# Kernel tuning notes

Hardware: AMD Instinct MI355X
Metric: run time of the kernel (lower is better)

## Reference

```python
import jax, jax.numpy as jnp
import numpy as np

FEAT_DIM = 256
NUM_HEADS = 4
GATE_HID = FEAT_DIM // 4
LN_EPS = 1e-5


def setup_inputs() -> dict:
    key = jax.random.key(0)
    ks = jax.random.split(key, 12)
    C, H = FEAT_DIM, NUM_HEADS
    s = 1.0 / np.sqrt(C)
    inp = {
        "features": jax.random.normal(ks[0], (8, 16384, C), dtype=jnp.float32),
        "view_proj_w": jax.random.normal(ks[1], (C, C), dtype=jnp.float32) * s,
        "view_proj_b": jnp.zeros((C,), dtype=jnp.float32),
        "in_proj_w": jax.random.normal(ks[2], (3 * C, C), dtype=jnp.float32) * s,
        "in_proj_b": jnp.zeros((3 * C,), dtype=jnp.float32),
        "out_proj_w": jax.random.normal(ks[3], (C, C), dtype=jnp.float32) * s,
        "out_proj_b": jnp.zeros((C,), dtype=jnp.float32),
        "gate_w1": jax.random.normal(ks[4], (GATE_HID, C), dtype=jnp.float32) * s,
        "gate_b1": jnp.zeros((GATE_HID,), dtype=jnp.float32),
        "gate_w2": jax.random.normal(ks[5], (1, GATE_HID), dtype=jnp.float32) * (1.0 / np.sqrt(GATE_HID)),
        "gate_b2": jnp.zeros((1,), dtype=jnp.float32),
        "ln_g": jnp.ones((C,), dtype=jnp.float32),
        "ln_b": jnp.zeros((C,), dtype=jnp.float32),
    }
    return inp


def reference(features, view_proj_w, view_proj_b, in_proj_w, in_proj_b,
              out_proj_w, out_proj_b, gate_w1, gate_b1, gate_w2, gate_b2,
              ln_g, ln_b):
    N, L, C = features.shape
    H = NUM_HEADS
    D = C // H

    # view embedding: scalar id/N broadcast over C, then Linear  -> [N,1,C]
    view_ids = (jnp.arange(N, dtype=features.dtype) / N)[:, None, None]  # [N,1,1]
    view_vec = jnp.broadcast_to(view_ids, (N, 1, C))
    view_info = view_vec @ view_proj_w.T + view_proj_b                    # [N,1,C]
    view_features = features + view_info                                  # [N,L,C]

    tokens = jnp.transpose(view_features, (1, 0, 2))                      # [L,N,C]

    # batched tiny cross-view self-attention: batch=L, seq=N
    qkv = tokens @ in_proj_w.T + in_proj_b                                # [L,N,3C]
    q, k, v = jnp.split(qkv, 3, axis=-1)
    q = q.reshape(L, N, H, D)
    k = k.reshape(L, N, H, D)
    v = v.reshape(L, N, H, D)
    scores = jnp.einsum("lnhd,lmhd->lhnm", q, k) / jnp.sqrt(jnp.array(D, features.dtype))
    attn = jax.nn.softmax(scores, axis=-1)                                # [L,H,N,N]
    ctx = jnp.einsum("lhnm,lmhd->lnhd", attn, v).reshape(L, N, C)
    attended = ctx @ out_proj_w.T + out_proj_b                            # [L,N,C]

    # gated softmax aggregation over views
    g = jax.nn.relu(attended @ gate_w1.T + gate_b1)                       # [L,N,C/4]
    g = jax.nn.sigmoid(g @ gate_w2.T + gate_b2)[..., 0]                   # [L,N]
    w = jax.nn.softmax(g, axis=-1)                                        # [L,N]
    fused = jnp.einsum("lnc,ln->lc", attended, w)[None]                   # [1,L,C]

    # LayerNorm over C
    mu = fused.mean(-1, keepdims=True)
    var = fused.var(-1, keepdims=True)
    fused = (fused - mu) * jax.lax.rsqrt(var + LN_EPS) * ln_g + ln_b
    return fused
```

## Files before the change

kernel.cpp:

```cpp
#include <hip/hip_runtime.h>

#define L_DIM 16384
#define C_DIM 256
#define NV 8
#define NH 4
#define DH 64
#define TL 4
#define NTHREADS 256

#define QKP 132
#define VVP 68
#define GPAD 68

typedef __attribute__((ext_vector_type(8))) _Float16 f16x8;
typedef __attribute__((ext_vector_type(4))) _Float16 f16x4;
typedef __attribute__((ext_vector_type(2))) _Float16 f16x2;
typedef __attribute__((ext_vector_type(4))) float f32x4;

union F8u { f16x8 v; f16x2 p[4]; };

__global__ void prep_kernel(const float* __restrict__ vw, const float* __restrict__ vb,
                            const float* __restrict__ w_in, const float* __restrict__ w_out,
                            const float* __restrict__ w_g1,
                            float* __restrict__ view_info, _Float16* __restrict__ win_pk,
                            _Float16* __restrict__ wout_pk, _Float16* __restrict__ wg1_pk){
  int tid = threadIdx.x, bid = blockIdx.x;
  if (bid == 0){
    int c = tid;
    const float4* vr = (const float4*)(vw + c*C_DIM);
    float rs = 0.f;
#pragma unroll 8
    for (int k = 0; k < 64; k++){ float4 x = vr[k]; rs += x.x + x.y + x.z + x.w; }
    float b = vb[c];
    for (int n = 0; n < NV; n++) view_info[n*C_DIM + c] = (n * 0.125f) * rs + b;
  }
  int gid = bid * blockDim.x + tid;
  int stride = gridDim.x * blockDim.x;
  const int NWIN = 24576, NWOUT = 8192, NWG = 2048;
  for (int f = gid; f < NWIN + NWOUT + NWG; f += stride){
    if (f < NWIN){
      int lane = f & 63, kc = (f>>6)&7, nt = (f>>9)&3, pc = f>>11;
      int p = pc % 3, h = pc / 3;
      int row = p*C_DIM + h*DH + nt*16 + (lane&15);
      int col = (lane>>4)*8 + kc*32;
      const float* src = w_in + (long)row*C_DIM + col;
      _Float16* d = win_pk + (long)f*8;
#pragma unroll
      for (int j = 0; j < 8; j++) d[j] = (_Float16)src[j];
    } else if (f < NWIN + NWOUT){
      int f2 = f - NWIN;
      int lane = f2 & 63, kc = (f2>>6)&7, nt = (f2>>9)&3, cc = f2>>11;
      int row = cc*64 + nt*16 + (lane&15);
      int col = (lane>>4)*8 + kc*32;
      const float* src = w_out + (long)row*C_DIM + col;
      _Float16* d = wout_pk + (long)f2*8;
#pragma unroll
      for (int j = 0; j < 8; j++) d[j] = (_Float16)src[j];
    } else {
      int f3 = f - NWIN - NWOUT;
      int lane = f3 & 63, kc = (f3>>6)&7, nt = (f3>>9)&3;
      int row = nt*16 + (lane&15);
      int col = (lane>>4)*8 + kc*32;
      const float* src = w_g1 + (long)row*C_DIM + col;
      _Float16* d = wg1_pk + (long)f3*8;
#pragma unroll
      for (int j = 0; j < 8; j++) d[j] = (_Float16)src[j];
    }
  }
}

__global__ __launch_bounds__(NTHREADS, 4)
void fused_kernel(const float* __restrict__ feat,
                  const float* __restrict__ view_info,
                  const _Float16* __restrict__ win,
                  const _Float16* __restrict__ wout,
                  const _Float16* __restrict__ wg1,
                  const float* __restrict__ b_in,
                  const float* __restrict__ b_out,
                  const float* __restrict__ b_g1,
                  const float* __restrict__ w2,
                  const float* __restrict__ b2,
                  const float* __restrict__ ln_g,
                  const float* __restrict__ ln_b,
                  float* __restrict__ out)
{
  extern __shared__ char smem[];
  _Float16* A   = (_Float16*)smem;
  _Float16* ctx = (_Float16*)smem;
  float*    g1s = (float*)smem;
  float* gl   = (float*)(smem + 8704);
  float* wgt  = gl + 32;
  float* red1 = wgt + 32;
  float* red2 = red1 + 128;
  float* mus  = red2 + 128;
  float* rvs  = mus + 4;
  _Float16* qk  = (_Float16*)(smem + 16384);
  _Float16* vv  = (_Float16*)(smem + 24832);
  _Float16* att = (_Float16*)(smem + 16384);

  const int tid  = threadIdx.x;
  const int wv   = tid >> 6, lane = tid & 63;
  const int quad = lane >> 4, l15 = lane & 15;

  const _Float16* wbin  = win  + (long)(wv*8)*512 + lane*8;
  const _Float16* wbout = wout + (long)(wv*32)*512 + lane*8;
  const _Float16* wbg1  = wg1  + (long)(wv*8)*512 + lane*8;

#define QSET(dst, g) do { int h_=(g)>>3, kc_=(g)&7; \
  dst[0] = *(const f16x8*)(wbin + ((h_*3+0)*32 + kc_)*512); \
  dst[1] = *(const f16x8*)(wbin + ((h_*3+1)*32 + kc_)*512); \
  dst[2] = *(const f16x8*)(wbin + ((h_*3+2)*32 + kc_)*512); } while(0)
#define OSET(dst, kc) do { \
  dst[0] = *(const f16x8*)(wbout + (0*8+(kc))*512); \
  dst[1] = *(const f16x8*)(wbout + (1*8+(kc))*512); \
  dst[2] = *(const f16x8*)(wbout + (2*8+(kc))*512); \
  dst[3] = *(const f16x8*)(wbout + (3*8+(kc))*512); } while(0)

  f16x8 wz[2][3];
  QSET(wz[0], 0);
  QSET(wz[1], 1);

  {
    int row = tid >> 3, j = tid & 7;
    int n = row & 7, lloc = row >> 3;
    long l = (long)blockIdx.x * TL + lloc;
    const float* fb = feat + ((long)n * L_DIM + l) * C_DIM + j*32;
    const float* vb = view_info + n * C_DIM + j*32;
    _Float16* arow = A + row*256;
#pragma unroll
    for (int i = 0; i < 4; i++){
      float4 x0 = *(const float4*)(fb + i*8);
      float4 x1 = *(const float4*)(fb + i*8 + 4);
      float4 v0 = *(const float4*)(vb + i*8);
      float4 v1 = *(const float4*)(vb + i*8 + 4);
      f16x8 hf;
      hf[0] = (_Float16)(x0.x+v0.x); hf[1] = (_Float16)(x0.y+v0.y);
      hf[2] = (_Float16)(x0.z+v0.z); hf[3] = (_Float16)(x0.w+v0.w);
      hf[4] = (_Float16)(x1.x+v1.x); hf[5] = (_Float16)(x1.y+v1.y);
      hf[6] = (_Float16)(x1.z+v1.z); hf[7] = (_Float16)(x1.w+v1.w);
      int s = j*4 + i;
      *(f16x8*)(arow + ((s ^ row))*8) = hf;
    }
  }
  __syncthreads();

  f16x8 wo[2][4];
  f16x8 wg[8];
  f16x8 cpk0, cpk1, cpk2;

#pragma unroll
  for (int h = 0; h < NH; h++){
    if (h) __syncthreads();
    {
      f32x4 z = {0.f,0.f,0.f,0.f};
      f32x4 acc[3][2];
#pragma unroll
      for (int p = 0; p < 3; p++){ acc[p][0] = z; acc[p][1] = z; }
#pragma unroll
      for (int kc = 0; kc < 8; kc++){
        int g = h*8 + kc;
        int s0 = quad + 4*kc;
        int r1 = 16 + l15;
        f16x8 a0 = *(const f16x8*)(A + l15*256 + ((s0 ^ l15))*8);
        f16x8 a1 = *(const f16x8*)(A + r1*256  + ((s0 ^ r1))*8);
#pragma unroll
        for (int p = 0; p < 3; p++){
          acc[p][0] = __builtin_amdgcn_mfma_f32_16x16x32_f16(wz[g&1][p], a0, acc[p][0], 0,0,0);
          acc[p][1] = __builtin_amdgcn_mfma_f32_16x16x32_f16(wz[g&1][p], a1, acc[p][1], 0,0,0);
        }
        if (g + 2 <= 31) QSET(wz[g&1], g+2);
      }
      int c4 = wv*16 + quad*4;
#pragma unroll
      for (int p = 0; p < 3; p++){
        float4 b4 = *(const float4*)(b_in + p*C_DIM + h*DH + c4);
        float bb[4] = {b4.x, b4.y, b4.z, b4.w};
        f16x4 s0, s1;
#pragma unroll
        for (int r = 0; r < 4; r++){
          s0[r] = (_Float16)(acc[p][0][r] + bb[r]);
          s1[r] = (_Float16)(acc[p][1][r] + bb[r]);
        }
        if (p < 2){
          *(f16x4*)(qk + l15*QKP      + p*64 + c4) = s0;
          *(f16x4*)(qk + (16+l15)*QKP + p*64 + c4) = s1;
        } else {
          *(f16x4*)(vv + l15*VVP      + c4) = s0;
          *(f16x4*)(vv + (16+l15)*VVP + c4) = s1;
        }
      }
    }
    __syncthreads();
    {
      if (h == 3){ OSET(wo[0], 0); OSET(wo[1], 1); }
      int nn = lane >> 3, mm = lane & 7;
      int tq = wv*8 + nn;
      const _Float16* qrow = qk + tq*QKP;
      const _Float16* krow = qk + (wv*8 + mm)*QKP + 64;
      float s = 0.f;
#pragma unroll
      for (int d8 = 0; d8 < 8; d8++){
        F8u q8, k8;
        q8.v = *(const f16x8*)(qrow + d8*8);
        k8.v = *(const f16x8*)(krow + d8*8);
#if __has_builtin(__builtin_amdgcn_fdot2)
#pragma unroll
        for (int j2 = 0; j2 < 4; j2++)
          s = __builtin_amdgcn_fdot2(q8.p[j2], k8.p[j2], s, false);
#else
#pragma unroll
        for (int j = 0; j < 8; j++) s += (float)q8.v[j] * (float)k8.v[j];
#endif
      }
      s *= 0.125f;
      float mx = s;
#pragma unroll
      for (int o = 1; o < 8; o <<= 1) mx = fmaxf(mx, __shfl_xor(mx, o));
      float e = __expf(s - mx);
      float sum = e;
#pragma unroll
      for (int o = 1; o < 8; o <<= 1) sum += __shfl_xor(sum, o);
      float attnw = e / sum;
      float c8[8] = {0,0,0,0,0,0,0,0};
#pragma unroll
      for (int mp = 0; mp < 8; mp++){
        float aw = __shfl(attnw, (nn<<3) | mp);
        f16x8 v8 = *(const f16x8*)(vv + (wv*8 + mp)*VVP + mm*8);
#pragma unroll
        for (int j = 0; j < 8; j++) c8[j] += aw * (float)v8[j];
      }
      f16x8 cp;
#pragma unroll
      for (int j = 0; j < 8; j++) cp[j] = (_Float16)c8[j];
      if (h == 0)      cpk0 = cp;
      else if (h == 1) cpk1 = cp;
      else if (h == 2) cpk2 = cp;
      else {
        _Float16* crow = ctx + tq*256;
        *(f16x8*)(crow + ((( 0 + mm) ^ tq))*8) = cpk0;
        *(f16x8*)(crow + ((( 8 + mm) ^ tq))*8) = cpk1;
        *(f16x8*)(crow + (((16 + mm) ^ tq))*8) = cpk2;
        *(f16x8*)(crow + (((24 + mm) ^ tq))*8) = cp;
      }
    }
  }
  __syncthreads();

  {
    f32x4 z = {0.f,0.f,0.f,0.f};
    f32x4 acc[4][2];
#pragma unroll
    for (int nt = 0; nt < 4; nt++){ acc[nt][0] = z; acc[nt][1] = z; }
#pragma unroll
    for (int kc = 0; kc < 8; kc++){
      int s0 = quad + 4*kc;
      int r1 = 16 + l15;
      f16x8 a0 = *(const f16x8*)(ctx + l15*256 + ((s0 ^ l15))*8);
      f16x8 a1 = *(const f16x8*)(ctx + r1*256  + ((s0 ^ r1))*8);
#pragma unroll
      for (int nt = 0; nt < 4; nt++){
        acc[nt][0] = __builtin_amdgcn_mfma_f32_16x16x32_f16(wo[kc&1][nt], a0, acc[nt][0], 0,0,0);
        acc[nt][1] = __builtin_amdgcn_mfma_f32_16x16x32_f16(wo[kc&1][nt], a1, acc[nt][1], 0,0,0);
      }
      if (kc < 6) OSET(wo[kc&1], kc+2);
    }
#pragma unroll
    for (int nt = 0; nt < 4; nt++){
      int c4 = wv*64 + nt*16 + quad*4;
      float4 b4 = *(const float4*)(b_out + c4);
      float bb[4] = {b4.x, b4.y, b4.z, b4.w};
      f16x4 s0, s1;
#pragma unroll
      for (int r = 0; r < 4; r++){
        s0[r] = (_Float16)(acc[nt][0][r] + bb[r]);
        s1[r] = (_Float16)(acc[nt][1][r] + bb[r]);
      }
      int slot = c4 >> 3, jo = c4 & 7;
      *(f16x4*)(att + l15*256      + ((slot ^ l15))*8      + jo) = s0;
      *(f16x4*)(att + (16+l15)*256 + ((slot ^ (16+l15)))*8 + jo) = s1;
    }
#pragma unroll
    for (int kc = 0; kc < 8; kc++) wg[kc] = *(const f16x8*)(wbg1 + kc*512);
  }
  __syncthreads();

  {
    f32x4 acc0 = {0.f,0.f,0.f,0.f}, acc1 = {0.f,0.f,0.f,0.f};
#pragma unroll
    for (int kc = 0; kc < 8; kc++){
      int s0 = quad + 4*kc;
      int r1 = 16 + l15;
      f16x8 a0 = *(const f16x8*)(att + l15*256 + ((s0 ^ l15))*8);
      f16x8 a1 = *(const f16x8*)(att + r1*256  + ((s0 ^ r1))*8);
      acc0 = __builtin_amdgcn_mfma_f32_16x16x32_f16(wg[kc], a0, acc0, 0,0,0);
      acc1 = __builtin_amdgcn_mfma_f32_16x16x32_f16(wg[kc], a1, acc1, 0,0,0);
    }
    int c4 = wv*16 + quad*4;
    float4 b4 = *(const float4*)(b_g1 + c4);
    float bb[4] = {b4.x, b4.y, b4.z, b4.w};
    float4 o0, o1;
    o0.x = fmaxf(acc0[0]+bb[0], 0.f); o0.y = fmaxf(acc0[1]+bb[1], 0.f);
    o0.z = fmaxf(acc0[2]+bb[2], 0.f); o0.w = fmaxf(acc0[3]+bb[3], 0.f);
    o1.x = fmaxf(acc1[0]+bb[0], 0.f); o1.y = fmaxf(acc1[1]+bb[1], 0.f);
    o1.z = fmaxf(acc1[2]+bb[2], 0.f); o1.w = fmaxf(acc1[3]+bb[3], 0.f);
    *(float4*)(g1s + l15*GPAD      + c4) = o0;
    *(float4*)(g1s + (16+l15)*GPAD + c4) = o1;
  }
  __syncthreads();

  {
    int t = tid >> 3, part = tid & 7;
    const float* g1r = g1s + t*GPAD + part*8;
    const float* w2p = w2 + part*8;
    float s = 0.f;
#pragma unroll
    for (int j = 0; j < 8; j++) s += g1r[j] * w2p[j];
    s += __shfl_xor(s, 1);
    s += __shfl_xor(s, 2);
    s += __shfl_xor(s, 4);
    if (part == 0) gl[t] = 1.f / (1.f + __expf(-(s + b2[0])));
  }
  __syncthreads();
  if (tid < 4){
    float v[8]; float mx = -1e30f;
    for (int n = 0; n < 8; n++){ v[n] = gl[tid*8+n]; mx = fmaxf(mx, v[n]); }
    float sum = 0.f;
    for (int n = 0; n < 8; n++){ v[n] = __expf(v[n]-mx); sum += v[n]; }
    float inv = 1.f/sum;
    for (int n = 0; n < 8; n++) wgt[tid*8+n] = v[n]*inv;
  }
  __syncthreads();

  float f8[8];
  const int lfl = tid >> 5, ccf = tid & 31;
  if (tid < 128){
    float wloc[8];
#pragma unroll
    for (int n = 0; n < 8; n++) wloc[n] = wgt[lfl*8+n];
#pragma unroll
    for (int j = 0; j < 8; j++) f8[j] = 0.f;
#pragma unroll
    for (int n = 0; n < 8; n++){
      int row = lfl*8 + n;
      f16x8 a8 = *(const f16x8*)(att + row*256 + ((ccf ^ row))*8);
      float aw = wloc[n];
#pragma unroll
      for (int j = 0; j < 8; j++) f8[j] += aw * (float)a8[j];
    }
    float s = 0.f, s2 = 0.f;
#pragma unroll
    for (int j = 0; j < 8; j++){ s += f8[j]; s2 += f8[j]*f8[j]; }
    red1[lfl*32 + ccf] = s;
    red2[lfl*32 + ccf] = s2;
  }
  __syncthreads();
  if (tid < 4){
    float s = 0.f, s2 = 0.f;
    for (int i = 0; i < 32; i++){ s += red1[tid*32+i]; s2 += red2[tid*32+i]; }
    float mu = s * (1.f/256.f);
    float var = s2 * (1.f/256.f) - mu*mu;
    mus[tid] = mu;
    rvs[tid] = rsqrtf(var + 1e-5f);
  }
  __syncthreads();
  if (tid < 128){
    float mu = mus[lfl], rv = rvs[lfl];
    long lg = (long)blockIdx.x * TL + lfl;
    float* op = out + lg * C_DIM + ccf*8;
    float o8[8];
#pragma unroll
    for (int j = 0; j < 8; j++){
      int c = ccf*8 + j;
      o8[j] = (f8[j]-mu)*rv*ln_g[c] + ln_b[c];
    }
    *(float4*)(op)   = make_float4(o8[0],o8[1],o8[2],o8[3]);
    *(float4*)(op+4) = make_float4(o8[4],o8[5],o8[6],o8[7]);
  }
}

extern "C" void kernel_launch(void* const* d_in, const int* in_sizes, int n_in,
                              void* d_out, int out_size, void* d_ws, size_t ws_size,
                              hipStream_t stream){
  const float* feat  = (const float*)d_in[0];
  const float* vw    = (const float*)d_in[1];
  const float* vb    = (const float*)d_in[2];
  const float* w_in  = (const float*)d_in[3];
  const float* b_in  = (const float*)d_in[4];
  const float* w_out = (const float*)d_in[5];
  const float* b_out = (const float*)d_in[6];
  const float* w_g1  = (const float*)d_in[7];
  const float* b_g1  = (const float*)d_in[8];
  const float* w2    = (const float*)d_in[9];
  const float* b2    = (const float*)d_in[10];
  const float* lng   = (const float*)d_in[11];
  const float* lnb   = (const float*)d_in[12];

  char* ws = (char*)d_ws;
  float*    view_info = (float*)ws;
  _Float16* win_pk  = (_Float16*)(ws + 8192);
  _Float16* wout_pk = (_Float16*)(ws + 401408);
  _Float16* wg1_pk  = (_Float16*)(ws + 532480);

  prep_kernel<<<256, 256, 0, stream>>>(vw, vb, w_in, w_out, w_g1,
                                       view_info, win_pk, wout_pk, wg1_pk);
  fused_kernel<<<L_DIM/TL, NTHREADS, 32768, stream>>>(
      feat, view_info, win_pk, wout_pk, wg1_pk,
      b_in, b_out, b_g1, w2, b2, lng, lnb, (float*)d_out);
}
```

Before: 434.9 us.

## Double tokens per block to 8 with 512 threads and two row-pair wave groups

Each block now handles 8 sequence positions (64 token rows) with 8 waves, split into two 32-row groups that share the same column-tile weight fragments. Shared memory doubles to 64 KB, and the swizzle is adjusted to use the row index modulo 32. The out-projection and gate weight loads move out of the attention loop into their own phases, with an extra barrier added. The goal is fewer blocks and better amortized weight fetches per block, at the cost of higher LDS use, which may reduce occupancy.

```diff
diff --git a/kernel.cpp b/kernel.cpp
--- a/kernel.cpp
+++ b/kernel.cpp
@@ -5,8 +5,8 @@
 #define NV 8
 #define NH 4
 #define DH 64
-#define TL 4
-#define NTHREADS 256
+#define TL 8
+#define NTHREADS 512
 
 #define QKP 132
 #define VVP 68
@@ -88,23 +88,26 @@
   _Float16* A   = (_Float16*)smem;
   _Float16* ctx = (_Float16*)smem;
   float*    g1s = (float*)smem;
-  float* gl   = (float*)(smem + 8704);
-  float* wgt  = gl + 32;
-  float* red1 = wgt + 32;
-  float* red2 = red1 + 128;
-  float* mus  = red2 + 128;
-  float* rvs  = mus + 4;
-  _Float16* qk  = (_Float16*)(smem + 16384);
-  _Float16* vv  = (_Float16*)(smem + 24832);
-  _Float16* att = (_Float16*)(smem + 16384);
+  float* gl   = (float*)(smem + 17408);
+  float* wgt  = gl + 64;
+  float* red1 = wgt + 64;
+  float* red2 = red1 + 256;
+  float* mus  = red2 + 256;
+  float* rvs  = mus + 8;
+  _Float16* qk  = (_Float16*)(smem + 32768);
+  _Float16* vv  = (_Float16*)(smem + 49664);
+  _Float16* att = (_Float16*)(smem + 32768);
 
   const int tid  = threadIdx.x;
   const int wv   = tid >> 6, lane = tid & 63;
   const int quad = lane >> 4, l15 = lane & 15;
-
-  const _Float16* wbin  = win  + (long)(wv*8)*512 + lane*8;
-  const _Float16* wbout = wout + (long)(wv*32)*512 + lane*8;
-  const _Float16* wbg1  = wg1  + (long)(wv*8)*512 + lane*8;
+  const int rp   = wv >> 2, ct = wv & 3;
+  const int r0   = rp*32 + l15;
+  const int r1   = rp*32 + 16 + l15;
+
+  const _Float16* wbin  = win  + (long)(ct*8)*512 + lane*8;
+  const _Float16* wbout = wout + (long)(ct*32)*512 + lane*8;
+  const _Float16* wbg1  = wg1  + (long)(ct*8)*512 + lane*8;
 
 #define QSET(dst, g) do { int h_=(g)>>3, kc_=(g)&7; \
   dst[0] = *(const f16x8*)(wbin + ((h_*3+0)*32 + kc_)*512); \
@@ -139,13 +142,11 @@
       hf[4] = (_Float16)(x1.x+v1.x); hf[5] = (_Float16)(x1.y+v1.y);
       hf[6] = (_Float16)(x1.z+v1.z); hf[7] = (_Float16)(x1.w+v1.w);
       int s = j*4 + i;
-      *(f16x8*)(arow + ((s ^ row))*8) = hf;
-    }
-  }
-  __syncthreads();
-
-  f16x8 wo[2][4];
-  f16x8 wg[8];
+      *(f16x8*)(arow + ((s ^ (row & 31)))*8) = hf;
+    }
+  }
+  __syncthreads();
+
   f16x8 cpk0, cpk1, cpk2;
 
 #pragma unroll
@@ -160,9 +161,8 @@
       for (int kc = 0; kc < 8; kc++){
         int g = h*8 + kc;
         int s0 = quad + 4*kc;
-        int r1 = 16 + l15;
-        f16x8 a0 = *(const f16x8*)(A + l15*256 + ((s0 ^ l15))*8);
-        f16x8 a1 = *(const f16x8*)(A + r1*256  + ((s0 ^ r1))*8);
+        f16x8 a0 = *(const f16x8*)(A + r0*256 + ((s0 ^ l15))*8);
+        f16x8 a1 = *(const f16x8*)(A + r1*256 + ((s0 ^ (16 + l15)))*8);
 #pragma unroll
         for (int p = 0; p < 3; p++){
           acc[p][0] = __builtin_amdgcn_mfma_f32_16x16x32_f16(wz[g&1][p], a0, acc[p][0], 0,0,0);
@@ -170,29 +170,28 @@
         }
         if (g + 2 <= 31) QSET(wz[g&1], g+2);
       }
-      int c4 = wv*16 + quad*4;
+      int c4 = ct*16 + quad*4;
 #pragma unroll
       for (int p = 0; p < 3; p++){
         float4 b4 = *(const float4*)(b_in + p*C_DIM + h*DH + c4);
         float bb[4] = {b4.x, b4.y, b4.z, b4.w};
-        f16x4 s0, s1;
+        f16x4 s0v, s1v;
 #pragma unroll
         for (int r = 0; r < 4; r++){
-          s0[r] = (_Float16)(acc[p][0][r] + bb[r]);
-          s1[r] = (_Float16)(acc[p][1][r] + bb[r]);
+          s0v[r] = (_Float16)(acc[p][0][r] + bb[r]);
+          s1v[r] = (_Float16)(acc[p][1][r] + bb[r]);
         }
         if (p < 2){
-          *(f16x4*)(qk + l15*QKP      + p*64 + c4) = s0;
-          *(f16x4*)(qk + (16+l15)*QKP + p*64 + c4) = s1;
+          *(f16x4*)(qk + r0*QKP + p*64 + c4) = s0v;
+          *(f16x4*)(qk + r1*QKP + p*64 + c4) = s1v;
         } else {
-          *(f16x4*)(vv + l15*VVP      + c4) = s0;
-          *(f16x4*)(vv + (16+l15)*VVP + c4) = s1;
+          *(f16x4*)(vv + r0*VVP + c4) = s0v;
+          *(f16x4*)(vv + r1*VVP + c4) = s1v;
         }
       }
     }
     __syncthreads();
     {
-      if (h == 3){ OSET(wo[0], 0); OSET(wo[1], 1); }
       int nn = lane >> 3, mm = lane & 7;
       int tq = wv*8 + nn;
       const _Float16* qrow = qk + tq*QKP;
@@ -237,16 +236,20 @@
       else if (h == 2) cpk2 = cp;
       else {
         _Float16* crow = ctx + tq*256;
-        *(f16x8*)(crow + ((( 0 + mm) ^ tq))*8) = cpk0;
-        *(f16x8*)(crow + ((( 8 + mm) ^ tq))*8) = cpk1;
-        *(f16x8*)(crow + (((16 + mm) ^ tq))*8) = cpk2;
-        *(f16x8*)(crow + (((24 + mm) ^ tq))*8) = cp;
+        int tm = tq & 31;
+        *(f16x8*)(crow + ((( 0 + mm) ^ tm))*8) = cpk0;
+        *(f16x8*)(crow + ((( 8 + mm) ^ tm))*8) = cpk1;
+        *(f16x8*)(crow + (((16 + mm) ^ tm))*8) = cpk2;
+        *(f16x8*)(crow + (((24 + mm) ^ tm))*8) = cp;
       }
     }
   }
   __syncthreads();
 
   {
+    f16x8 wo[2][4];
+    OSET(wo[0], 0);
+    OSET(wo[1], 1);
     f32x4 z = {0.f,0.f,0.f,0.f};
     f32x4 acc[4][2];
 #pragma unroll
@@ -254,9 +257,8 @@
 #pragma unroll
     for (int kc = 0; kc < 8; kc++){
       int s0 = quad + 4*kc;
-      int r1 = 16 + l15;
-      f16x8 a0 = *(const f16x8*)(ctx + l15*256 + ((s0 ^ l15))*8);
-      f16x8 a1 = *(const f16x8*)(ctx + r1*256  + ((s0 ^ r1))*8);
+      f16x8 a0 = *(const f16x8*)(ctx + r0*256 + ((s0 ^ l15))*8);
+      f16x8 a1 = *(const f16x8*)(ctx + r1*256 + ((s0 ^ (16 + l15)))*8);
 #pragma unroll
       for (int nt = 0; nt < 4; nt++){
         acc[nt][0] = __builtin_amdgcn_mfma_f32_16x16x32_f16(wo[kc&1][nt], a0, acc[nt][0], 0,0,0);
@@ -264,38 +266,39 @@
       }
       if (kc < 6) OSET(wo[kc&1], kc+2);
     }
+    __syncthreads();
 #pragma unroll
     for (int nt = 0; nt < 4; nt++){
-      int c4 = wv*64 + nt*16 + quad*4;
+      int c4 = ct*64 + nt*16 + quad*4;
       float4 b4 = *(const float4*)(b_out + c4);
       float bb[4] = {b4.x, b4.y, b4.z, b4.w};
-      f16x4 s0, s1;
+      f16x4 s0v, s1v;
 #pragma unroll
       for (int r = 0; r < 4; r++){
-        s0[r] = (_Float16)(acc[nt][0][r] + bb[r]);
-        s1[r] = (_Float16)(acc[nt][1][r] + bb[r]);
+        s0v[r] = (_Float16)(acc[nt][0][r] + bb[r]);
+        s1v[r] = (_Float16)(acc[nt][1][r] + bb[r]);
       }
       int slot = c4 >> 3, jo = c4 & 7;
-      *(f16x4*)(att + l15*256      + ((slot ^ l15))*8      + jo) = s0;
-      *(f16x4*)(att + (16+l15)*256 + ((slot ^ (16+l15)))*8 + jo) = s1;
-    }
+      *(f16x4*)(att + r0*256 + ((slot ^ l15))*8        + jo) = s0v;
+      *(f16x4*)(att + r1*256 + ((slot ^ (16 + l15)))*8 + jo) = s1v;
+    }
+  }
+  __syncthreads();
+
+  {
+    f16x8 wg[8];
 #pragma unroll
     for (int kc = 0; kc < 8; kc++) wg[kc] = *(const f16x8*)(wbg1 + kc*512);
-  }
-  __syncthreads();
-
-  {
     f32x4 acc0 = {0.f,0.f,0.f,0.f}, acc1 = {0.f,0.f,0.f,0.f};
 #pragma unroll
     for (int kc = 0; kc < 8; kc++){
       int s0 = quad + 4*kc;
-      int r1 = 16 + l15;
-      f16x8 a0 = *(const f16x8*)(att + l15*256 + ((s0 ^ l15))*8);
-      f16x8 a1 = *(const f16x8*)(att + r1*256  + ((s0 ^ r1))*8);
+      f16x8 a0 = *(const f16x8*)(att + r0*256 + ((s0 ^ l15))*8);
+      f16x8 a1 = *(const f16x8*)(att + r1*256 + ((s0 ^ (16 + l15)))*8);
       acc0 = __builtin_amdgcn_mfma_f32_16x16x32_f16(wg[kc], a0, acc0, 0,0,0);
       acc1 = __builtin_amdgcn_mfma_f32_16x16x32_f16(wg[kc], a1, acc1, 0,0,0);
     }
-    int c4 = wv*16 + quad*4;
+    int c4 = ct*16 + quad*4;
     float4 b4 = *(const float4*)(b_g1 + c4);
     float bb[4] = {b4.x, b4.y, b4.z, b4.w};
     float4 o0, o1;
@@ -303,8 +306,8 @@
     o0.z = fmaxf(acc0[2]+bb[2], 0.f); o0.w = fmaxf(acc0[3]+bb[3], 0.f);
     o1.x = fmaxf(acc1[0]+bb[0], 0.f); o1.y = fmaxf(acc1[1]+bb[1], 0.f);
     o1.z = fmaxf(acc1[2]+bb[2], 0.f); o1.w = fmaxf(acc1[3]+bb[3], 0.f);
-    *(float4*)(g1s + l15*GPAD      + c4) = o0;
-    *(float4*)(g1s + (16+l15)*GPAD + c4) = o1;
+    *(float4*)(g1s + r0*GPAD + c4) = o0;
+    *(float4*)(g1s + r1*GPAD + c4) = o1;
   }
   __syncthreads();
 
@@ -321,19 +324,22 @@
     if (part == 0) gl[t] = 1.f / (1.f + __expf(-(s + b2[0])));
   }
   __syncthreads();
-  if (tid < 4){
+  if (tid < 8){
     float v[8]; float mx = -1e30f;
+#pragma unroll
     for (int n = 0; n < 8; n++){ v[n] = gl[tid*8+n]; mx = fmaxf(mx, v[n]); }
     float sum = 0.f;
+#pragma unroll
     for (int n = 0; n < 8; n++){ v[n] = __expf(v[n]-mx); sum += v[n]; }
     float inv = 1.f/sum;
+#pragma unroll
     for (int n = 0; n < 8; n++) wgt[tid*8+n] = v[n]*inv;
   }
   __syncthreads();
 
   float f8[8];
   const int lfl = tid >> 5, ccf = tid & 31;
-  if (tid < 128){
+  if (tid < 256){
     float wloc[8];
 #pragma unroll
     for (int n = 0; n < 8; n++) wloc[n] = wgt[lfl*8+n];
@@ -342,7 +348,7 @@
 #pragma unroll
     for (int n = 0; n < 8; n++){
       int row = lfl*8 + n;
-      f16x8 a8 = *(const f16x8*)(att + row*256 + ((ccf ^ row))*8);
+      f16x8 a8 = *(const f16x8*)(att + row*256 + ((ccf ^ (row & 31)))*8);
       float aw = wloc[n];
 #pragma unroll
       for (int j = 0; j < 8; j++) f8[j] += aw * (float)a8[j];
@@ -354,7 +360,7 @@
     red2[lfl*32 + ccf] = s2;
   }
   __syncthreads();
-  if (tid < 4){
+  if (tid < 8){
     float s = 0.f, s2 = 0.f;
     for (int i = 0; i < 32; i++){ s += red1[tid*32+i]; s2 += red2[tid*32+i]; }
     float mu = s * (1.f/256.f);
@@ -363,7 +369,7 @@
     rvs[tid] = rsqrtf(var + 1e-5f);
   }
   __syncthreads();
-  if (tid < 128){
+  if (tid < 256){
     float mu = mus[lfl], rv = rvs[lfl];
     long lg = (long)blockIdx.x * TL + lfl;
     float* op = out + lg * C_DIM + ccf*8;
@@ -403,7 +409,7 @@
 
   prep_kernel<<<256, 256, 0, stream>>>(vw, vb, w_in, w_out, w_g1,
                                        view_info, win_pk, wout_pk, wg1_pk);
-  fused_kernel<<<L_DIM/TL, NTHREADS, 32768, stream>>>(
+  fused_kernel<<<L_DIM/TL, NTHREADS, 65536, stream>>>(
       feat, view_info, win_pk, wout_pk, wg1_pk,
       b_in, b_out, b_g1, w2, b2, lng, lnb, (float*)d_out);
 }
```

After: 457.5 us. +5.2%, slower.

## Split GEMM phases into smaller register working sets to raise occupancy

Applied to the files above, without the earlier changes.

Raises the launch-bounds occupancy hint from 4 to 5 blocks per CU. To fit that, the fused QKV projection is split into a Q/K pass and a separate V pass, and the output projection into two halves. Weight prefetching is limited to a local double buffer instead of carrying weights across phases, and the gate weights are no longer preloaded into eight registers. This lowers live registers at the cost of reading the A/ctx LDS tiles more times and losing cross-phase weight prefetch overlap.

```diff
diff --git a/kernel.cpp b/kernel.cpp
--- a/kernel.cpp
+++ b/kernel.cpp
@@ -69,7 +69,7 @@
   }
 }
 
-__global__ __launch_bounds__(NTHREADS, 4)
+__global__ __launch_bounds__(NTHREADS, 5)
 void fused_kernel(const float* __restrict__ feat,
                   const float* __restrict__ view_info,
                   const _Float16* __restrict__ win,
@@ -106,19 +106,13 @@
   const _Float16* wbout = wout + (long)(wv*32)*512 + lane*8;
   const _Float16* wbg1  = wg1  + (long)(wv*8)*512 + lane*8;
 
-#define QSET(dst, g) do { int h_=(g)>>3, kc_=(g)&7; \
-  dst[0] = *(const f16x8*)(wbin + ((h_*3+0)*32 + kc_)*512); \
-  dst[1] = *(const f16x8*)(wbin + ((h_*3+1)*32 + kc_)*512); \
-  dst[2] = *(const f16x8*)(wbin + ((h_*3+2)*32 + kc_)*512); } while(0)
-#define OSET(dst, kc) do { \
-  dst[0] = *(const f16x8*)(wbout + (0*8+(kc))*512); \
-  dst[1] = *(const f16x8*)(wbout + (1*8+(kc))*512); \
-  dst[2] = *(const f16x8*)(wbout + (2*8+(kc))*512); \
-  dst[3] = *(const f16x8*)(wbout + (3*8+(kc))*512); } while(0)
-
-  f16x8 wz[2][3];
-  QSET(wz[0], 0);
-  QSET(wz[1], 1);
+#define WQK(dst, h_, kc_) do { \
+  dst[0] = *(const f16x8*)(wbin + (((h_)*3+0)*32 + (kc_))*512); \
+  dst[1] = *(const f16x8*)(wbin + (((h_)*3+1)*32 + (kc_))*512); } while(0)
+#define WVLD(h_, kc_) (*(const f16x8*)(wbin + (((h_)*3+2)*32 + (kc_))*512))
+#define WOUT2(dst, ntb, kc_) do { \
+  dst[0] = *(const f16x8*)(wbout + (((ntb)+0)*8 + (kc_))*512); \
+  dst[1] = *(const f16x8*)(wbout + (((ntb)+1)*8 + (kc_))*512); } while(0)
 
   {
     int row = tid >> 3, j = tid & 7;
@@ -144,8 +138,6 @@
   }
   __syncthreads();
 
-  f16x8 wo[2][4];
-  f16x8 wg[8];
   f16x8 cpk0, cpk1, cpk2;
 
 #pragma unroll
@@ -153,46 +145,67 @@
     if (h) __syncthreads();
     {
       f32x4 z = {0.f,0.f,0.f,0.f};
-      f32x4 acc[3][2];
-#pragma unroll
-      for (int p = 0; p < 3; p++){ acc[p][0] = z; acc[p][1] = z; }
+      f32x4 acc00=z, acc01=z, acc10=z, acc11=z;
+      f16x8 wa[2][2];
+      WQK(wa[0], h, 0);
+      WQK(wa[1], h, 1);
 #pragma unroll
       for (int kc = 0; kc < 8; kc++){
-        int g = h*8 + kc;
         int s0 = quad + 4*kc;
         int r1 = 16 + l15;
         f16x8 a0 = *(const f16x8*)(A + l15*256 + ((s0 ^ l15))*8);
         f16x8 a1 = *(const f16x8*)(A + r1*256  + ((s0 ^ r1))*8);
-#pragma unroll
-        for (int p = 0; p < 3; p++){
-          acc[p][0] = __builtin_amdgcn_mfma_f32_16x16x32_f16(wz[g&1][p], a0, acc[p][0], 0,0,0);
-          acc[p][1] = __builtin_amdgcn_mfma_f32_16x16x32_f16(wz[g&1][p], a1, acc[p][1], 0,0,0);
-        }
-        if (g + 2 <= 31) QSET(wz[g&1], g+2);
+        acc00 = __builtin_amdgcn_mfma_f32_16x16x32_f16(wa[kc&1][0], a0, acc00, 0,0,0);
+        acc01 = __builtin_amdgcn_mfma_f32_16x16x32_f16(wa[kc&1][0], a1, acc01, 0,0,0);
+        acc10 = __builtin_amdgcn_mfma_f32_16x16x32_f16(wa[kc&1][1], a0, acc10, 0,0,0);
+        acc11 = __builtin_amdgcn_mfma_f32_16x16x32_f16(wa[kc&1][1], a1, acc11, 0,0,0);
+        if (kc < 6) WQK(wa[kc&1], h, kc+2);
       }
       int c4 = wv*16 + quad*4;
 #pragma unroll
-      for (int p = 0; p < 3; p++){
+      for (int p = 0; p < 2; p++){
         float4 b4 = *(const float4*)(b_in + p*C_DIM + h*DH + c4);
         float bb[4] = {b4.x, b4.y, b4.z, b4.w};
-        f16x4 s0, s1;
+        f16x4 s0v, s1v;
 #pragma unroll
         for (int r = 0; r < 4; r++){
-          s0[r] = (_Float16)(acc[p][0][r] + bb[r]);
-          s1[r] = (_Float16)(acc[p][1][r] + bb[r]);
+          s0v[r] = (_Float16)((p ? acc10[r] : acc00[r]) + bb[r]);
+          s1v[r] = (_Float16)((p ? acc11[r] : acc01[r]) + bb[r]);
         }
-        if (p < 2){
-          *(f16x4*)(qk + l15*QKP      + p*64 + c4) = s0;
-          *(f16x4*)(qk + (16+l15)*QKP + p*64 + c4) = s1;
-        } else {
-          *(f16x4*)(vv + l15*VVP      + c4) = s0;
-          *(f16x4*)(vv + (16+l15)*VVP + c4) = s1;
-        }
-      }
+        *(f16x4*)(qk + l15*QKP      + p*64 + c4) = s0v;
+        *(f16x4*)(qk + (16+l15)*QKP + p*64 + c4) = s1v;
+      }
+    }
+    {
+      f32x4 z = {0.f,0.f,0.f,0.f};
+      f32x4 acc20=z, acc21=z;
+      f16x8 wb0 = WVLD(h, 0);
+      f16x8 wb1 = WVLD(h, 1);
+#pragma unroll
+      for (int kc = 0; kc < 8; kc++){
+        int s0 = quad + 4*kc;
+        int r1 = 16 + l15;
+        f16x8 a0 = *(const f16x8*)(A + l15*256 + ((s0 ^ l15))*8);
+        f16x8 a1 = *(const f16x8*)(A + r1*256  + ((s0 ^ r1))*8);
+        f16x8 w = (kc & 1) ? wb1 : wb0;
+        acc20 = __builtin_amdgcn_mfma_f32_16x16x32_f16(w, a0, acc20, 0,0,0);
+        acc21 = __builtin_amdgcn_mfma_f32_16x16x32_f16(w, a1, acc21, 0,0,0);
+        if (kc < 6){ if (kc & 1) wb1 = WVLD(h, kc+2); else wb0 = WVLD(h, kc+2); }
+      }
+      int c4 = wv*16 + quad*4;
+      float4 b4 = *(const float4*)(b_in + 2*C_DIM + h*DH + c4);
+      float bb[4] = {b4.x, b4.y, b4.z, b4.w};
+      f16x4 s0v, s1v;
+#pragma unroll
+      for (int r = 0; r < 4; r++){
+        s0v[r] = (_Float16)(acc20[r] + bb[r]);
+        s1v[r] = (_Float16)(acc21[r] + bb[r]);
+      }
+      *(f16x4*)(vv + l15*VVP      + c4) = s0v;
+      *(f16x4*)(vv + (16+l15)*VVP + c4) = s1v;
     }
     __syncthreads();
     {
-      if (h == 3){ OSET(wo[0], 0); OSET(wo[1], 1); }
       int nn = lane >> 3, mm = lane & 7;
       int tq = wv*8 + nn;
       const _Float16* qrow = qk + tq*QKP;
@@ -246,11 +259,14 @@
   }
   __syncthreads();
 
-  {
+#pragma unroll
+  for (int half = 0; half < 2; half++){
+    int ntb = half*2;
     f32x4 z = {0.f,0.f,0.f,0.f};
-    f32x4 acc[4][2];
-#pragma unroll
-    for (int nt = 0; nt < 4; nt++){ acc[nt][0] = z; acc[nt][1] = z; }
+    f32x4 acc0[2] = {z, z}, acc1[2] = {z, z};
+    f16x8 wo[2][2];
+    WOUT2(wo[0], ntb, 0);
+    WOUT2(wo[1], ntb, 1);
 #pragma unroll
     for (int kc = 0; kc < 8; kc++){
       int s0 = quad + 4*kc;
@@ -258,42 +274,47 @@
       f16x8 a0 = *(const f16x8*)(ctx + l15*256 + ((s0 ^ l15))*8);
       f16x8 a1 = *(const f16x8*)(ctx + r1*256  + ((s0 ^ r1))*8);
 #pragma unroll
-      for (int nt = 0; nt < 4; nt++){
-        acc[nt][0] = __builtin_amdgcn_mfma_f32_16x16x32_f16(wo[kc&1][nt], a0, acc[nt][0], 0,0,0);
-        acc[nt][1] = __builtin_amdgcn_mfma_f32_16x16x32_f16(wo[kc&1][nt], a1, acc[nt][1], 0,0,0);
-      }
-      if (kc < 6) OSET(wo[kc&1], kc+2);
-    }
-#pragma unroll
-    for (int nt = 0; nt < 4; nt++){
-      int c4 = wv*64 + nt*16 + quad*4;
+      for (int i = 0; i < 2; i++){
+        acc0[i] = __builtin_amdgcn_mfma_f32_16x16x32_f16(wo[kc&1][i], a0, acc0[i], 0,0,0);
+        acc1[i] = __builtin_amdgcn_mfma_f32_16x16x32_f16(wo[kc&1][i], a1, acc1[i], 0,0,0);
+      }
+      if (kc < 6) WOUT2(wo[kc&1], ntb, kc+2);
+    }
+#pragma unroll
+    for (int i = 0; i < 2; i++){
+      int c4 = wv*64 + (ntb+i)*16 + quad*4;
       float4 b4 = *(const float4*)(b_out + c4);
       float bb[4] = {b4.x, b4.y, b4.z, b4.w};
-      f16x4 s0, s1;
+      f16x4 s0v, s1v;
 #pragma unroll
       for (int r = 0; r < 4; r++){
-        s0[r] = (_Float16)(acc[nt][0][r] + bb[r]);
-        s1[r] = (_Float16)(acc[nt][1][r] + bb[r]);
+        s0v[r] = (_Float16)(acc0[i][r] + bb[r]);
+        s1v[r] = (_Float16)(acc1[i][r] + bb[r]);
       }
       int slot = c4 >> 3, jo = c4 & 7;
-      *(f16x4*)(att + l15*256      + ((slot ^ l15))*8      + jo) = s0;
-      *(f16x4*)(att + (16+l15)*256 + ((slot ^ (16+l15)))*8 + jo) = s1;
-    }
-#pragma unroll
-    for (int kc = 0; kc < 8; kc++) wg[kc] = *(const f16x8*)(wbg1 + kc*512);
+      *(f16x4*)(att + l15*256      + ((slot ^ l15))*8      + jo) = s0v;
+      *(f16x4*)(att + (16+l15)*256 + ((slot ^ (16+l15)))*8 + jo) = s1v;
+    }
   }
   __syncthreads();
 
   {
     f32x4 acc0 = {0.f,0.f,0.f,0.f}, acc1 = {0.f,0.f,0.f,0.f};
+    f16x8 wg0 = *(const f16x8*)(wbg1);
+    f16x8 wg1f = *(const f16x8*)(wbg1 + 512);
 #pragma unroll
     for (int kc = 0; kc < 8; kc++){
       int s0 = quad + 4*kc;
       int r1 = 16 + l15;
       f16x8 a0 = *(const f16x8*)(att + l15*256 + ((s0 ^ l15))*8);
       f16x8 a1 = *(const f16x8*)(att + r1*256  + ((s0 ^ r1))*8);
-      acc0 = __builtin_amdgcn_mfma_f32_16x16x32_f16(wg[kc], a0, acc0, 0,0,0);
-      acc1 = __builtin_amdgcn_mfma_f32_16x16x32_f16(wg[kc], a1, acc1, 0,0,0);
+      f16x8 w = (kc & 1) ? wg1f : wg0;
+      acc0 = __builtin_amdgcn_mfma_f32_16x16x32_f16(w, a0, acc0, 0,0,0);
+      acc1 = __builtin_amdgcn_mfma_f32_16x16x32_f16(w, a1, acc1, 0,0,0);
+      if (kc < 6){
+        if (kc & 1) wg1f = *(const f16x8*)(wbg1 + (kc+2)*512);
+        else        wg0  = *(const f16x8*)(wbg1 + (kc+2)*512);
+      }
     }
     int c4 = wv*16 + quad*4;
     float4 b4 = *(const float4*)(b_g1 + c4);
```

Result: slower. 527.3 us (+21.3%).
